# Optimization experiments

Measured on AMD Instinct MI355X. Metric: run time of the kernel, lower is better.

The kernel has to match this reference:

```python
import jax, jax.numpy as jnp
import numpy as np

HIDDEN = 1024
N_HEADS = 16
HEAD_DIM = HIDDEN // N_HEADS


def setup_inputs() -> dict:
    key = jax.random.key(0)
    ks = jax.random.split(key, 8)
    bs, seq = 8, 1024
    hidden_states = jax.random.normal(ks[0], (bs, seq, HIDDEN), dtype=jnp.float32)
    attention_mask = jnp.zeros((bs, 1, 1, seq), dtype=jnp.float32)
    s = 1.0 / np.sqrt(HIDDEN)
    Wq = jax.random.normal(ks[1], (HIDDEN, HIDDEN), dtype=jnp.float32) * s
    bq = jnp.zeros((HIDDEN,), dtype=jnp.float32)
    Wk = jax.random.normal(ks[2], (HIDDEN, HIDDEN), dtype=jnp.float32) * s
    bk = jnp.zeros((HIDDEN,), dtype=jnp.float32)
    Wv = jax.random.normal(ks[3], (HIDDEN, HIDDEN), dtype=jnp.float32) * s
    bv = jnp.zeros((HIDDEN,), dtype=jnp.float32)
    return {"hidden_states": hidden_states, "attention_mask": attention_mask,
            "Wq": Wq, "bq": bq, "Wk": Wk, "bk": bk, "Wv": Wv, "bv": bv}


def _split_heads(x):
    # [b, s, H] -> [b, h, s, d]
    b, s, _ = x.shape
    return x.reshape(b, s, N_HEADS, HEAD_DIM).transpose(0, 2, 1, 3)


def reference(hidden_states, attention_mask, Wq, bq, Wk, bk, Wv, bv):
    q = _split_heads(hidden_states @ Wq.T + bq)
    k = _split_heads(hidden_states @ Wk.T + bk)
    v = _split_heads(hidden_states @ Wv.T + bv)
    scale = 1.0 / np.sqrt(HEAD_DIM).astype(np.float32)
    scores = jnp.einsum('bhqd,bhkd->bhqk', q, k) * scale + attention_mask
    probs = jax.nn.softmax(scores, axis=-1)  # dropout p=0.0 -> identity
    ctx = jnp.einsum('bhqk,bhkd->bhqd', probs, v)
    b, h, s, d = ctx.shape
    return ctx.transpose(0, 2, 1, 3).reshape(b, s, h * d)
```

## Files before the change

kernel.cpp:

```cpp
#include <hip/hip_runtime.h>
#include <stdint.h>
#include <stddef.h>

#define HIDDEN 1024
#define NHEADS 16
#define HDIM   64
#define BS     8
#define SEQ    1024
#define MTOT   (BS*SEQ)
#define QKV_T  ((size_t)MTOT*HIDDEN)

typedef short    bf16x8 __attribute__((ext_vector_type(8)));
typedef float    f32x4  __attribute__((ext_vector_type(4)));
typedef uint16_t u16x4  __attribute__((ext_vector_type(4)));

__device__ __forceinline__ uint16_t f2bf(float f) {
  union { float f; uint32_t u; } c; c.f = f;
  uint32_t u = c.u + 0x7FFFu + ((c.u >> 16) & 1u);
  return (uint16_t)(u >> 16);
}

__device__ __forceinline__ uint32_t cvt_pk_bf16(float lo, float hi) {
  uint32_t r;
  asm("v_cvt_pk_bf16_f32 %0, %1, %2" : "=v"(r) : "v"(lo), "v"(hi));
  return r;
}

__device__ __forceinline__ float exp2fast(float x) {
#if __has_builtin(__builtin_amdgcn_exp2f)
  return __builtin_amdgcn_exp2f(x);
#else
  return __expf(x * 0.69314718056f);
#endif
}

__device__ __forceinline__ void gload_lds16(const uint16_t* g, uint16_t* lds) {
  __builtin_amdgcn_global_load_lds(
      (const __attribute__((address_space(1))) uint32_t*)g,
      (__attribute__((address_space(3))) uint32_t*)lds, 16, 0, 0);
}

__global__ __launch_bounds__(256) void cvt_kernel(
    const float* __restrict__ hs, const float* __restrict__ wq,
    const float* __restrict__ wk, const float* __restrict__ wv,
    uint16_t* __restrict__ hsb, uint16_t* __restrict__ wcat)
{
  const int i4 = blockIdx.x * 256 + threadIdx.x;
  f32x4 v;
  u16x4 o;
  if (i4 < 2097152) {
    v = *((const f32x4*)hs + i4);
    o[0]=f2bf(v[0]); o[1]=f2bf(v[1]); o[2]=f2bf(v[2]); o[3]=f2bf(v[3]);
    *((u16x4*)hsb + i4) = o;
  } else {
    int j4 = i4 - 2097152;
    int w  = j4 >> 18;
    int r4 = j4 & 262143;
    const float* src = (w == 0) ? wq : ((w == 1) ? wk : wv);
    v = *((const f32x4*)src + r4);
    o[0]=f2bf(v[0]); o[1]=f2bf(v[1]); o[2]=f2bf(v[2]); o[3]=f2bf(v[3]);
    *((u16x4*)wcat + j4) = o;
  }
}

__global__ __launch_bounds__(256) void gemm_qkv(
    const uint16_t* __restrict__ hsb, const uint16_t* __restrict__ wcat,
    const float* __restrict__ bq, const float* __restrict__ bk,
    const float* __restrict__ bv, uint16_t* __restrict__ qbuf,
    uint16_t* __restrict__ kbuf, uint16_t* __restrict__ vtbuf)
{
  __shared__ uint16_t Alds[2][128*32];
  __shared__ uint16_t Blds[2][128*32];

  const int bid = blockIdx.x;
  const int wg  = (bid & 7) * 192 + (bid >> 3);
  const int tm  = wg / 24, tn = wg % 24;
  const int m0  = tm * 128, n0 = tn * 128;
  const int t   = threadIdx.x;
  const int l   = t & 63, w = t >> 6;
  const int wm  = w >> 1, wn = w & 1;

  f32x4 acc[4][4];
#pragma unroll
  for (int i = 0; i < 4; i++)
#pragma unroll
    for (int j = 0; j < 4; j++) acc[i][j] = (f32x4){0.f,0.f,0.f,0.f};

  const int r0   = (w * 2) * 16 + (l >> 2);
  const int r1   = (w * 2 + 1) * 16 + (l >> 2);
  const int g0s  = (l & 3) ^ ((r0 >> 1) & 3);
  const int g1s  = (l & 3) ^ ((r1 >> 1) & 3);
  const size_t aoff0 = (size_t)r0 * HIDDEN + g0s * 8;
  const size_t aoff1 = (size_t)r1 * HIDDEN + g1s * 8;

  auto STAGE = [&](int buf, int kt) {
    const uint16_t* Ab = hsb  + (size_t)m0 * HIDDEN + kt * 32;
    const uint16_t* Bb = wcat + (size_t)n0 * HIDDEN + kt * 32;
    gload_lds16(Ab + aoff0, &Alds[buf][(w * 2) * 512]);
    gload_lds16(Ab + aoff1, &Alds[buf][(w * 2 + 1) * 512]);
    gload_lds16(Bb + aoff0, &Blds[buf][(w * 2) * 512]);
    gload_lds16(Bb + aoff1, &Blds[buf][(w * 2 + 1) * 512]);
  };

  auto COMPUTE = [&](int buf) {
    bf16x8 af[4], bfr[4];
    const int G = l >> 4;
#pragma unroll
    for (int i = 0; i < 4; i++) {
      int ar = wm * 64 + i * 16 + (l & 15);
      int gs = (G ^ ((ar >> 1) & 3)) & 3;
      af[i] = *(const bf16x8*)&Alds[buf][ar * 32 + gs * 8];
    }
#pragma unroll
    for (int j = 0; j < 4; j++) {
      int br = wn * 64 + j * 16 + (l & 15);
      int gs = (G ^ ((br >> 1) & 3)) & 3;
      bfr[j] = *(const bf16x8*)&Blds[buf][br * 32 + gs * 8];
    }
#pragma unroll
    for (int i = 0; i < 4; i++)
#pragma unroll
      for (int j = 0; j < 4; j++)
        acc[i][j] = __builtin_amdgcn_mfma_f32_16x16x32_bf16(af[i], bfr[j], acc[i][j], 0, 0, 0);
  };

  STAGE(0, 0);
  __syncthreads();
#pragma unroll 1
  for (int kt = 0; kt < 32; ++kt) {
    int cur = kt & 1;
    if (kt < 31) STAGE(cur ^ 1, kt + 1);
    COMPUTE(cur);
    __syncthreads();
  }

#pragma unroll
  for (int j = 0; j < 4; j++) {
    int n     = n0 + wn * 64 + j * 16 + (l & 15);
    int which = n >> 10, nn = n & 1023;
    const float* bp = (which == 0) ? bq : ((which == 1) ? bk : bv);
    float bias = bp[nn];
    int hh = nn >> 6, dd = nn & 63;
#pragma unroll
    for (int i = 0; i < 4; i++) {
      if (which == 2) {
        int m_  = m0 + wm * 64 + i * 16 + (l >> 4) * 4;
        int b_  = m_ >> 10, s_ = m_ & 1023;
        size_t bhh = (size_t)(b_ * NHEADS + hh);
        uint2 pk;
        pk.x = cvt_pk_bf16(acc[i][j][0] + bias, acc[i][j][1] + bias);
        pk.y = cvt_pk_bf16(acc[i][j][2] + bias, acc[i][j][3] + bias);
        *(uint2*)&vtbuf[(bhh * HDIM + dd) * SEQ + s_] = pk;
      } else {
#pragma unroll
        for (int r = 0; r < 4; r++) {
          int m  = m0 + wm * 64 + i * 16 + (l >> 4) * 4 + r;
          int b_ = m >> 10, s_ = m & 1023;
          float val = acc[i][j][r] + bias;
          size_t bhh = (size_t)(b_ * NHEADS + hh);
          if (which == 0)
            qbuf[(bhh * SEQ + s_) * HDIM + dd] = f2bf(val * 0.18033688011112042f);
          else
            kbuf[(bhh * SEQ + s_) * HDIM + dd] = f2bf(val);
        }
      }
    }
  }
}

__global__ __launch_bounds__(256) void attn_kernel(
    const uint16_t* __restrict__ qb, const uint16_t* __restrict__ kb,
    const uint16_t* __restrict__ vtb, const float* __restrict__ mask,
    float* __restrict__ out)
{
  __shared__ uint16_t Klds[64 * 64];
  __shared__ uint16_t Vlds[64 * 64];
  __shared__ uint16_t Plds[4][32 * 64];
  __shared__ float    mlds[SEQ];

  const int bid = blockIdx.x;
  const int wg  = (bid & 7) * 128 + (bid >> 3);
  const int bh  = wg >> 3;
  const int qt  = wg & 7;
  const int b   = bh >> 4, h = bh & 15;

  const uint16_t* Qg = qb  + (size_t)bh * SEQ * HDIM;
  const uint16_t* Kg = kb  + (size_t)bh * SEQ * HDIM;
  const uint16_t* Vg = vtb + (size_t)bh * HDIM * SEQ;

  const int t = threadIdx.x, l = t & 63, w = t >> 6;
  const int G = l >> 4, q16 = l & 15;

  for (int i = t; i < SEQ; i += 256)
    mlds[i] = mask[b * SEQ + i] * 1.44269504089f;

  const int q0w = qt * 128 + w * 32;
  bf16x8 qf[2][2];
#pragma unroll
  for (int qi = 0; qi < 2; ++qi)
#pragma unroll
    for (int k0 = 0; k0 < 2; ++k0)
      qf[qi][k0] = *(const bf16x8*)(Qg + (size_t)(q0w + qi * 16 + q16) * HDIM + k0 * 32 + G * 8);

  f32x4 O[4][2];
#pragma unroll
  for (int dt = 0; dt < 4; dt++) { O[dt][0] = (f32x4){0,0,0,0}; O[dt][1] = (f32x4){0,0,0,0}; }
  float mrow[2] = {-3e38f, -3e38f}, lrow[2] = {0.f, 0.f};

  __syncthreads();

  const int srow8 = l >> 3;
  const int gsrc  = (l & 7) ^ srow8;
  uint16_t* Pw = &Plds[w][0];
  const int qsw = q16 & 7;

#pragma unroll 1
  for (int kt = 0; kt < 16; ++kt) {
#pragma unroll
    for (int ia = 0; ia < 2; ia++) {
      const int rbase = ia * 32 + w * 8;
      const int row   = rbase + srow8;
      gload_lds16(Kg + (size_t)(kt * 64 + row) * HDIM + gsrc * 8, &Klds[rbase * 64]);
      gload_lds16(Vg + (size_t)row * SEQ + kt * 64 + gsrc * 8,    &Vlds[rbase * 64]);
    }
    __syncthreads();

    f32x4 mv[4];
#pragma unroll
    for (int jn = 0; jn < 4; jn++)
      mv[jn] = *(const f32x4*)&mlds[kt * 64 + jn * 16 + G * 4];

#pragma unroll
    for (int qi = 0; qi < 2; ++qi) {
      f32x4 sc[4];
#pragma unroll
      for (int jn = 0; jn < 4; jn++) sc[jn] = (f32x4){0,0,0,0};
#pragma unroll
      for (int k0 = 0; k0 < 2; ++k0)
#pragma unroll
        for (int jn = 0; jn < 4; jn++) {
          int kr = jn * 16 + q16;
          int gs = ((k0 * 4 + G) ^ qsw) & 7;
          bf16x8 kf = *(const bf16x8*)&Klds[kr * 64 + gs * 8];
          sc[jn] = __builtin_amdgcn_mfma_f32_16x16x32_bf16(kf, qf[qi][k0], sc[jn], 0, 0, 0);
        }

      float pm = -3e38f;
#pragma unroll
      for (int jn = 0; jn < 4; jn++) {
        sc[jn] += mv[jn];
        pm = fmaxf(pm, fmaxf(fmaxf(sc[jn][0], sc[jn][1]), fmaxf(sc[jn][2], sc[jn][3])));
      }
      pm = fmaxf(pm, __shfl_xor(pm, 16));
      pm = fmaxf(pm, __shfl_xor(pm, 32));
      if (!__all(pm <= mrow[qi] + 11.0f)) {
        float mn = fmaxf(mrow[qi], pm);
        float fs = exp2fast(mrow[qi] - mn);
        mrow[qi] = mn;
        lrow[qi] *= fs;
#pragma unroll
        for (int dt = 0; dt < 4; dt++) O[dt][qi] *= fs;
      }
      float ps = 0.f;
      const int q = qi * 16 + q16;
#pragma unroll
      for (int jn = 0; jn < 4; jn++) {
        float p0 = exp2fast(sc[jn][0] - mrow[qi]);
        float p1 = exp2fast(sc[jn][1] - mrow[qi]);
        float p2 = exp2fast(sc[jn][2] - mrow[qi]);
        float p3 = exp2fast(sc[jn][3] - mrow[qi]);
        ps += (p0 + p1) + (p2 + p3);
        uint2 pw2;
        pw2.x = cvt_pk_bf16(p0, p1);
        pw2.y = cvt_pk_bf16(p2, p3);
        int g16 = (jn * 2 + (G >> 1)) ^ qsw;
        *(uint2*)&Pw[q * 64 + g16 * 8 + (G & 1) * 4] = pw2;
      }
      ps += __shfl_xor(ps, 16);
      ps += __shfl_xor(ps, 32);
      lrow[qi] += ps;
    }

#pragma unroll
    for (int ks = 0; ks < 2; ++ks) {
      int gp  = ks * 4 + G;
      int gsp = (gp ^ qsw) & 7;
      bf16x8 pf0 = *(const bf16x8*)&Pw[(q16     ) * 64 + gsp * 8];
      bf16x8 pf1 = *(const bf16x8*)&Pw[(16 + q16) * 64 + gsp * 8];
#pragma unroll
      for (int dt = 0; dt < 4; dt++) {
        int dr = dt * 16 + q16;
        bf16x8 vf = *(const bf16x8*)&Vlds[dr * 64 + gsp * 8];
        O[dt][0] = __builtin_amdgcn_mfma_f32_16x16x32_bf16(vf, pf0, O[dt][0], 0, 0, 0);
        O[dt][1] = __builtin_amdgcn_mfma_f32_16x16x32_bf16(vf, pf1, O[dt][1], 0, 0, 0);
      }
    }
    __syncthreads();
  }

#pragma unroll
  for (int qi = 0; qi < 2; ++qi) {
    float inv = 1.0f / lrow[qi];
    int q = q0w + qi * 16 + q16;
    float* orow = out + (size_t)(b * SEQ + q) * HIDDEN + h * HDIM;
#pragma unroll
    for (int dt = 0; dt < 4; dt++) {
      f32x4 o4 = O[dt][qi] * inv;
      *(f32x4*)(orow + dt * 16 + G * 4) = o4;
    }
  }
}

extern "C" void kernel_launch(void* const* d_in, const int* in_sizes, int n_in,
                              void* d_out, int out_size, void* d_ws, size_t ws_size,
                              hipStream_t stream) {
  const float* hs   = (const float*)d_in[0];
  const float* mask = (const float*)d_in[1];
  const float* Wq   = (const float*)d_in[2];
  const float* bq   = (const float*)d_in[3];
  const float* Wk   = (const float*)d_in[4];
  const float* bk   = (const float*)d_in[5];
  const float* Wv   = (const float*)d_in[6];
  const float* bv   = (const float*)d_in[7];
  float* out = (float*)d_out;

  uint16_t* hsb  = (uint16_t*)d_ws;
  uint16_t* wcat = (uint16_t*)((char*)d_ws + 16777216u);
  uint16_t* qbuf = (uint16_t*)((char*)d_ws + 23068672u);
  uint16_t* kbuf = (uint16_t*)((char*)d_ws + 39845888u);
  uint16_t* vtbf = (uint16_t*)((char*)d_ws + 56623104u);

  cvt_kernel<<<11264, 256, 0, stream>>>(hs, Wq, Wk, Wv, hsb, wcat);
  gemm_qkv<<<1536, 256, 0, stream>>>(hsb, wcat, bq, bk, bv, qbuf, kbuf, vtbf);
  attn_kernel<<<1024, 256, 0, stream>>>(qbuf, kbuf, vtbf, mask, out);
}
```

Baseline: 148.7 us.

## Double-buffer K/V tiles in attention kernel to overlap loads with compute

Allocates two LDS buffers for K and V and issues the direct-to-LDS global loads for the next key tile before computing on the current one, with a vmcnt wait and barrier at the end of each iteration. K fragments are also hoisted into registers once per tile and reused for both query sub-tiles instead of being reloaded from LDS. This aims to hide global load latency behind the MFMA and softmax work, at the cost of twice the K/V LDS footprint and more live registers, which may reduce occupancy.

```diff
diff --git a/kernel.cpp b/kernel.cpp
--- a/kernel.cpp
+++ b/kernel.cpp
@@ -173,8 +173,8 @@
     const uint16_t* __restrict__ vtb, const float* __restrict__ mask,
     float* __restrict__ out)
 {
-  __shared__ uint16_t Klds[64 * 64];
-  __shared__ uint16_t Vlds[64 * 64];
+  __shared__ uint16_t Klds[2][64 * 64];
+  __shared__ uint16_t Vlds[2][64 * 64];
   __shared__ uint16_t Plds[4][32 * 64];
   __shared__ float    mlds[SEQ];
 
@@ -207,29 +207,44 @@
   for (int dt = 0; dt < 4; dt++) { O[dt][0] = (f32x4){0,0,0,0}; O[dt][1] = (f32x4){0,0,0,0}; }
   float mrow[2] = {-3e38f, -3e38f}, lrow[2] = {0.f, 0.f};
 
-  __syncthreads();
-
   const int srow8 = l >> 3;
   const int gsrc  = (l & 7) ^ srow8;
   uint16_t* Pw = &Plds[w][0];
   const int qsw = q16 & 7;
 
-#pragma unroll 1
-  for (int kt = 0; kt < 16; ++kt) {
+  auto STAGE = [&](int buf, int kt2) {
 #pragma unroll
     for (int ia = 0; ia < 2; ia++) {
       const int rbase = ia * 32 + w * 8;
       const int row   = rbase + srow8;
-      gload_lds16(Kg + (size_t)(kt * 64 + row) * HDIM + gsrc * 8, &Klds[rbase * 64]);
-      gload_lds16(Vg + (size_t)row * SEQ + kt * 64 + gsrc * 8,    &Vlds[rbase * 64]);
-    }
-    __syncthreads();
+      gload_lds16(Kg + (size_t)(kt2 * 64 + row) * HDIM + gsrc * 8, &Klds[buf][rbase * 64]);
+      gload_lds16(Vg + (size_t)row * SEQ + kt2 * 64 + gsrc * 8,    &Vlds[buf][rbase * 64]);
+    }
+  };
+
+  STAGE(0, 0);
+  __syncthreads();
+
+#pragma unroll 1
+  for (int kt = 0; kt < 16; ++kt) {
+    const int cur = kt & 1;
+    if (kt < 15) STAGE(cur ^ 1, kt + 1);
 
     f32x4 mv[4];
 #pragma unroll
     for (int jn = 0; jn < 4; jn++)
       mv[jn] = *(const f32x4*)&mlds[kt * 64 + jn * 16 + G * 4];
 
+    bf16x8 kf[2][4];
+#pragma unroll
+    for (int k0 = 0; k0 < 2; ++k0)
+#pragma unroll
+      for (int jn = 0; jn < 4; jn++) {
+        int kr = jn * 16 + q16;
+        int gs = ((k0 * 4 + G) ^ qsw) & 7;
+        kf[k0][jn] = *(const bf16x8*)&Klds[cur][kr * 64 + gs * 8];
+      }
+
 #pragma unroll
     for (int qi = 0; qi < 2; ++qi) {
       f32x4 sc[4];
@@ -238,12 +253,8 @@
 #pragma unroll
       for (int k0 = 0; k0 < 2; ++k0)
 #pragma unroll
-        for (int jn = 0; jn < 4; jn++) {
-          int kr = jn * 16 + q16;
-          int gs = ((k0 * 4 + G) ^ qsw) & 7;
-          bf16x8 kf = *(const bf16x8*)&Klds[kr * 64 + gs * 8];
-          sc[jn] = __builtin_amdgcn_mfma_f32_16x16x32_bf16(kf, qf[qi][k0], sc[jn], 0, 0, 0);
-        }
+        for (int jn = 0; jn < 4; jn++)
+          sc[jn] = __builtin_amdgcn_mfma_f32_16x16x32_bf16(kf[k0][jn], qf[qi][k0], sc[jn], 0, 0, 0);
 
       float pm = -3e38f;
 #pragma unroll
@@ -290,12 +301,17 @@
 #pragma unroll
       for (int dt = 0; dt < 4; dt++) {
         int dr = dt * 16 + q16;
-        bf16x8 vf = *(const bf16x8*)&Vlds[dr * 64 + gsp * 8];
+        bf16x8 vf = *(const bf16x8*)&Vlds[cur][dr * 64 + gsp * 8];
         O[dt][0] = __builtin_amdgcn_mfma_f32_16x16x32_bf16(vf, pf0, O[dt][0], 0, 0, 0);
         O[dt][1] = __builtin_amdgcn_mfma_f32_16x16x32_bf16(vf, pf1, O[dt][1], 0, 0, 0);
       }
     }
-    __syncthreads();
+
+    if (kt < 15) {
+      asm volatile("s_waitcnt vmcnt(0)" ::: "memory");
+      __builtin_amdgcn_s_barrier();
+      __builtin_amdgcn_sched_barrier(0);
+    }
   }
 
 #pragma unroll
```

Result: no change. 150.7 us (+1.3%).

## Deepen QKV GEMM prefetch and register-prefetch K/V tiles in attention

Applied to the files above, without the earlier changes.

In the QKV projection GEMM, two LDS stages are now loaded before the loop. Each iteration waits with a partial vmcnt so the tile two steps ahead stays in flight while the current tile is computed, replacing full __syncthreads with raw barriers. In the attention kernel, the next K/V tile is loaded into registers at the start of each iteration and written into the swizzled LDS layout after compute, so the global load latency overlaps with the MFMA work. This trades extra VGPR pressure and hand-tuned waitcnt assumptions for less exposed memory latency.

```diff
diff --git a/kernel.cpp b/kernel.cpp
--- a/kernel.cpp
+++ b/kernel.cpp
@@ -125,13 +125,19 @@
   };
 
   STAGE(0, 0);
-  __syncthreads();
+  STAGE(1, 1);
 #pragma unroll 1
   for (int kt = 0; kt < 32; ++kt) {
-    int cur = kt & 1;
-    if (kt < 31) STAGE(cur ^ 1, kt + 1);
-    COMPUTE(cur);
-    __syncthreads();
+    if (kt < 31) { asm volatile("s_waitcnt vmcnt(4)" ::: "memory"); }
+    else         { asm volatile("s_waitcnt vmcnt(0)" ::: "memory"); }
+    __builtin_amdgcn_s_barrier();
+    __builtin_amdgcn_sched_barrier(0);
+    COMPUTE(kt & 1);
+    if (kt < 31) {
+      __builtin_amdgcn_s_barrier();
+      __builtin_amdgcn_sched_barrier(0);
+      if (kt < 30) STAGE(kt & 1, kt + 2);
+    }
   }
 
 #pragma unroll
@@ -207,23 +213,32 @@
   for (int dt = 0; dt < 4; dt++) { O[dt][0] = (f32x4){0,0,0,0}; O[dt][1] = (f32x4){0,0,0,0}; }
   float mrow[2] = {-3e38f, -3e38f}, lrow[2] = {0.f, 0.f};
 
-  __syncthreads();
-
   const int srow8 = l >> 3;
   const int gsrc  = (l & 7) ^ srow8;
+  const int slotw = (l & 7);
   uint16_t* Pw = &Plds[w][0];
   const int qsw = q16 & 7;
 
+#pragma unroll
+  for (int ia = 0; ia < 2; ia++) {
+    const int rbase = ia * 32 + w * 8;
+    const int row   = rbase + srow8;
+    gload_lds16(Kg + (size_t)row * HDIM + gsrc * 8,  &Klds[rbase * 64]);
+    gload_lds16(Vg + (size_t)row * SEQ + gsrc * 8,   &Vlds[rbase * 64]);
+  }
+  __syncthreads();
+
 #pragma unroll 1
   for (int kt = 0; kt < 16; ++kt) {
-#pragma unroll
-    for (int ia = 0; ia < 2; ia++) {
-      const int rbase = ia * 32 + w * 8;
-      const int row   = rbase + srow8;
-      gload_lds16(Kg + (size_t)(kt * 64 + row) * HDIM + gsrc * 8, &Klds[rbase * 64]);
-      gload_lds16(Vg + (size_t)row * SEQ + kt * 64 + gsrc * 8,    &Vlds[rbase * 64]);
-    }
-    __syncthreads();
+    bf16x8 kpre[2], vpre[2];
+    if (kt < 15) {
+#pragma unroll
+      for (int ia = 0; ia < 2; ia++) {
+        const int row = ia * 32 + w * 8 + srow8;
+        kpre[ia] = *(const bf16x8*)(Kg + (size_t)((kt + 1) * 64 + row) * HDIM + (l & 7) * 8);
+        vpre[ia] = *(const bf16x8*)(Vg + (size_t)row * SEQ + (kt + 1) * 64 + (l & 7) * 8);
+      }
+    }
 
     f32x4 mv[4];
 #pragma unroll
@@ -295,7 +310,21 @@
         O[dt][1] = __builtin_amdgcn_mfma_f32_16x16x32_bf16(vf, pf1, O[dt][1], 0, 0, 0);
       }
     }
-    __syncthreads();
+
+    if (kt < 15) {
+      __builtin_amdgcn_s_barrier();
+      __builtin_amdgcn_sched_barrier(0);
+#pragma unroll
+      for (int ia = 0; ia < 2; ia++) {
+        const int rbase = ia * 32 + w * 8;
+        const int row   = rbase + srow8;
+        *(bf16x8*)&Klds[row * 64 + gsrc * 8] = kpre[ia];
+        *(bf16x8*)&Vlds[row * 64 + gsrc * 8] = vpre[ia];
+      }
+      asm volatile("s_waitcnt lgkmcnt(0)" ::: "memory");
+      __builtin_amdgcn_s_barrier();
+      __builtin_amdgcn_sched_barrier(0);
+    }
   }
 
 #pragma unroll
```

Measured after the change: 150.2 us. Within noise of the previous version (+1.0%).

## Keep attention probabilities in registers and deepen GEMM prefetch pipeline

Applied to the files above, without the earlier changes.

In the attention kernel, the softmax probabilities are packed straight into bf16x4 register fragments and fed to 16x16x16 MFMAs. This removes the per-wave P round trip through LDS and the LDS staging buffer for it, at the cost of twice as many smaller MFMA instructions. Separately, the projection GEMM now issues two stages ahead and uses explicit vmcnt waits with raw barriers instead of __syncthreads. The goal is to overlap global loads with compute more deeply.

```diff
diff --git a/kernel.cpp b/kernel.cpp
--- a/kernel.cpp
+++ b/kernel.cpp
@@ -11,6 +11,7 @@
 #define QKV_T  ((size_t)MTOT*HIDDEN)
 
 typedef short    bf16x8 __attribute__((ext_vector_type(8)));
+typedef short    bf16x4 __attribute__((ext_vector_type(4)));
 typedef float    f32x4  __attribute__((ext_vector_type(4)));
 typedef uint16_t u16x4  __attribute__((ext_vector_type(4)));
 
@@ -24,6 +25,26 @@
   uint32_t r;
   asm("v_cvt_pk_bf16_f32 %0, %1, %2" : "=v"(r) : "v"(lo), "v"(hi));
   return r;
+}
+
+__device__ __forceinline__ bf16x4 pack_bf16x4(float a, float b, float c, float d) {
+  union { uint2 u; bf16x4 v; } cv;
+  cv.u.x = cvt_pk_bf16(a, b);
+  cv.u.y = cvt_pk_bf16(c, d);
+  return cv.v;
+}
+
+__device__ __forceinline__ f32x4 mfma_16x16x16(bf16x4 a, bf16x4 b, f32x4 c) {
+#if __has_builtin(__builtin_amdgcn_mfma_f32_16x16x16bf16_1k)
+  return __builtin_amdgcn_mfma_f32_16x16x16bf16_1k(a, b, c, 0, 0, 0);
+#elif __has_builtin(__builtin_amdgcn_mfma_f32_16x16x16_bf16)
+  return __builtin_amdgcn_mfma_f32_16x16x16_bf16(a, b, c, 0, 0, 0);
+#else
+  f32x4 d;
+  asm("v_mfma_f32_16x16x16_bf16 %0, %1, %2, %3"
+      : "=&v"(d) : "v"(a), "v"(b), "v"(c));
+  return d;
+#endif
 }
 
 __device__ __forceinline__ float exp2fast(float x) {
@@ -125,13 +146,19 @@
   };
 
   STAGE(0, 0);
-  __syncthreads();
+  STAGE(1, 1);
 #pragma unroll 1
   for (int kt = 0; kt < 32; ++kt) {
-    int cur = kt & 1;
-    if (kt < 31) STAGE(cur ^ 1, kt + 1);
-    COMPUTE(cur);
-    __syncthreads();
+    if (kt < 31) { asm volatile("s_waitcnt vmcnt(4)" ::: "memory"); }
+    else         { asm volatile("s_waitcnt vmcnt(0)" ::: "memory"); }
+    __builtin_amdgcn_s_barrier();
+    __builtin_amdgcn_sched_barrier(0);
+    COMPUTE(kt & 1);
+    if (kt < 31) {
+      __builtin_amdgcn_s_barrier();
+      __builtin_amdgcn_sched_barrier(0);
+      if (kt < 30) STAGE(kt & 1, kt + 2);
+    }
   }
 
 #pragma unroll
@@ -175,7 +202,6 @@
 {
   __shared__ uint16_t Klds[64 * 64];
   __shared__ uint16_t Vlds[64 * 64];
-  __shared__ uint16_t Plds[4][32 * 64];
   __shared__ float    mlds[SEQ];
 
   const int bid = blockIdx.x;
@@ -207,12 +233,11 @@
   for (int dt = 0; dt < 4; dt++) { O[dt][0] = (f32x4){0,0,0,0}; O[dt][1] = (f32x4){0,0,0,0}; }
   float mrow[2] = {-3e38f, -3e38f}, lrow[2] = {0.f, 0.f};
 
-  __syncthreads();
-
   const int srow8 = l >> 3;
   const int gsrc  = (l & 7) ^ srow8;
-  uint16_t* Pw = &Plds[w][0];
   const int qsw = q16 & 7;
+
+  __syncthreads();
 
 #pragma unroll 1
   for (int kt = 0; kt < 16; ++kt) {
@@ -229,6 +254,8 @@
 #pragma unroll
     for (int jn = 0; jn < 4; jn++)
       mv[jn] = *(const f32x4*)&mlds[kt * 64 + jn * 16 + G * 4];
+
+    bf16x4 pa[2][4];
 
 #pragma unroll
     for (int qi = 0; qi < 2; ++qi) {
@@ -262,7 +289,6 @@
         for (int dt = 0; dt < 4; dt++) O[dt][qi] *= fs;
       }
       float ps = 0.f;
-      const int q = qi * 16 + q16;
 #pragma unroll
       for (int jn = 0; jn < 4; jn++) {
         float p0 = exp2fast(sc[jn][0] - mrow[qi]);
@@ -270,11 +296,7 @@
         float p2 = exp2fast(sc[jn][2] - mrow[qi]);
         float p3 = exp2fast(sc[jn][3] - mrow[qi]);
         ps += (p0 + p1) + (p2 + p3);
-        uint2 pw2;
-        pw2.x = cvt_pk_bf16(p0, p1);
-        pw2.y = cvt_pk_bf16(p2, p3);
-        int g16 = (jn * 2 + (G >> 1)) ^ qsw;
-        *(uint2*)&Pw[q * 64 + g16 * 8 + (G & 1) * 4] = pw2;
+        pa[qi][jn] = pack_bf16x4(p0, p1, p2, p3);
       }
       ps += __shfl_xor(ps, 16);
       ps += __shfl_xor(ps, 32);
@@ -282,17 +304,15 @@
     }
 
 #pragma unroll
-    for (int ks = 0; ks < 2; ++ks) {
-      int gp  = ks * 4 + G;
-      int gsp = (gp ^ qsw) & 7;
-      bf16x8 pf0 = *(const bf16x8*)&Pw[(q16     ) * 64 + gsp * 8];
-      bf16x8 pf1 = *(const bf16x8*)&Pw[(16 + q16) * 64 + gsp * 8];
+    for (int jn = 0; jn < 4; jn++) {
+      const int gq = 2 * jn + (G >> 1);
 #pragma unroll
       for (int dt = 0; dt < 4; dt++) {
-        int dr = dt * 16 + q16;
-        bf16x8 vf = *(const bf16x8*)&Vlds[dr * 64 + gsp * 8];
-        O[dt][0] = __builtin_amdgcn_mfma_f32_16x16x32_bf16(vf, pf0, O[dt][0], 0, 0, 0);
-        O[dt][1] = __builtin_amdgcn_mfma_f32_16x16x32_bf16(vf, pf1, O[dt][1], 0, 0, 0);
+        const int dr   = dt * 16 + q16;
+        const int slot = gq ^ (dr & 7);
+        bf16x4 vf = *(const bf16x4*)&Vlds[dr * 64 + slot * 8 + (G & 1) * 4];
+        O[dt][0] = mfma_16x16x16(vf, pa[0][jn], O[dt][0]);
+        O[dt][1] = mfma_16x16x16(vf, pa[1][jn], O[dt][1]);
       }
     }
     __syncthreads();
```

Result: no change. 151.5 us (+1.9%).
